# Optimization experiments

Measured on AMD Instinct MI355X. Metric: run time of the kernel, lower is better.

## Reference

```python
import jax, jax.numpy as jnp
import numpy as np
from jax.scipy.special import logsumexp

# ---- static hyperparameters (from init_kwargs) ----
NG, NF, NW = 5, 10, 4
STEP = NG + NF + 1            # 16 signatures per writer mini-batch
T, D_FEAT = 512, 64           # sequence length, embedding dim
N = NW * STEP                 # 64 sequences in the batch
GAMMA = 5.0                   # soft-DTW gamma (bandwidth=0.1 -> int 0 -> no band)
MARGIN, ALPHA, BETA = 1.0, 0.1, 1.0
P_W, R_W = 0.1, 0.1
K_NUM, K_MUL = 5, 2.0
BIG = 1e10                    # stand-in for +inf in the DP boundary


def setup_inputs() -> dict:
    key = jax.random.key(0)
    k1, k2 = jax.random.split(key)
    data = jax.random.normal(k1, (N, T, D_FEAT), dtype=jnp.float32)
    lens = jax.random.randint(k2, (N,), T // 2, T + 1).astype(jnp.int32)
    return {"data": data, "lens": lens}


def _softdtw_batch(A, B, la, lb):
    """Batched soft-DTW (squared-Euclidean cost, softmin with gamma).
    A, B: (P, T, d); la, lb: (P,) int lengths. Returns R[la, lb] per pair.
    Anti-diagonal wavefront scan: diagonal k holds R[i, k-i]."""
    P = A.shape[0]
    a2 = jnp.sum(A * A, -1)
    b2 = jnp.sum(B * B, -1)
    Dm = a2[:, :, None] + b2[:, None, :] - 2.0 * jnp.einsum('ptd,psd->pts', A, B)  # (P,T,T)
    i_idx = jnp.arange(T + 1)
    r0 = jnp.broadcast_to(jnp.where(i_idx == 0, 0.0, BIG), (P, T + 1))  # diag k=0: R[0,0]=0
    r1 = jnp.full((P, T + 1), BIG, dtype=A.dtype)                        # diag k=1: boundary inf

    def shift(x):  # x[i] -> x[i-1], pad row i=0 with BIG
        return jnp.concatenate([jnp.full((P, 1), BIG, x.dtype), x[:, :-1]], axis=1)

    def step(carry, k):
        p2, p1 = carry          # diagonals k-2, k-1, each (P, T+1) indexed by i
        j = k - i_idx
        valid = (i_idx >= 1) & (j >= 1) & (j <= T)
        di = jnp.clip(i_idx - 1, 0, T - 1)
        dj = jnp.clip(j - 1, 0, T - 1)
        cost = Dm[:, di, dj]    # (P, T+1)
        # softmin over (R[i-1,j-1], R[i-1,j], R[i,j-1])
        stack = jnp.stack([shift(p2), shift(p1), p1], 0)
        smin = -GAMMA * logsumexp(-stack / GAMMA, axis=0)
        cur = jnp.where(valid[None, :], cost + smin, BIG)
        return (p1, cur), cur

    ks = jnp.arange(2, 2 * T + 1)
    _, ys = jax.lax.scan(step, (r0, r1), ks)  # (2T-1, P, T+1)
    return ys[la + lb - 2, jnp.arange(P), la]


def _mmd_pair(X, Y):
    """Multi-kernel Gaussian MMD between X, Y: (n, F) each."""
    n = X.shape[0]
    total = jnp.concatenate([X, Y], 0)
    sq = jnp.sum(total * total, -1)
    L2 = sq[:, None] + sq[None, :] - 2.0 * total @ total.T
    m = total.shape[0]
    bw = jnp.sum(L2) / (m * m - m)
    bw = bw / (K_MUL ** (K_NUM // 2))
    bws = bw * (K_MUL ** jnp.arange(K_NUM, dtype=X.dtype))
    K = jnp.sum(jnp.exp(-L2[None, :, :] / bws[:, None, None]), 0)
    return (jnp.mean(K[:n, :n]) + jnp.mean(K[n:, n:])
            - jnp.mean(K[:n, n:]) - jnp.mean(K[n:, :n]))


def _forward(data, lens):
    half = NF // 2
    # all anchor/(positive|negative) pairs across writers, flattened: P = NW*(NG+NF)
    a_idx, b_idx = [], []
    for w in range(NW):
        base = w * STEP
        for j in range(1, STEP):
            a_idx.append(base)
            b_idx.append(base + j)
    a_idx = jnp.array(a_idx)
    b_idx = jnp.array(b_idx)
    la, lb = lens[a_idx], lens[b_idx]
    raw = _softdtw_batch(data[a_idx], data[b_idx], la, lb)
    dist = (raw / (la + lb).astype(data.dtype)).reshape(NW, NG + NF)
    dist_g, dist_n = dist[:, :NG], dist[:, NG:]
    dk = jnp.sqrt(jnp.abs(jnp.mean(dist_g, 1)))       # (NW,)
    dg = dist_g / dk[:, None]
    dn = dist_n / dk[:, None]
    lk_s = jax.nn.relu(dg[:, :, None] + MARGIN - dn[:, None, :half])
    lk_r = jax.nn.relu(dg[:, :, None] + MARGIN - dn[:, None, half:])
    ca = jnp.mean(dg, 1)
    cb = jnp.mean(dn[:, :half], 1)
    intra = jnp.sum(dg - ca[:, None], 1)
    inter = jax.nn.relu(BETA - jnp.abs(ca - cb))
    cnt = jax.lax.stop_gradient(
        (jnp.sum(lk_s > 0, (1, 2)) + jnp.sum(lk_r > 0, (1, 2))).astype(data.dtype))
    lv = (jnp.sum(lk_s, (1, 2)) + jnp.sum(lk_r, (1, 2))) / (cnt + 1.0)
    total_loss = jnp.mean(lv + intra * P_W + inter * R_W)

    # pairwise MMD over writer mini-batches (first 1+NG+half signatures each)
    src, tgt = [], []
    for i in range(NW):
        for j in range(1, NW):
            if i != j:
                src.append(np.arange(STEP * i, STEP * (i + 1) - half))
                tgt.append(np.arange(STEP * j, STEP * (j + 1) - half))
    src = jnp.array(np.stack(src))
    tgt = jnp.array(np.stack(tgt))
    Xs = data[src].reshape(src.shape[0], src.shape[1], -1)  # flatten (T,d) per signature
    Ys = data[tgt].reshape(tgt.shape[0], tgt.shape[1], -1)
    mmds = jax.vmap(_mmd_pair)(Xs, Ys)
    siz = NW * (NW + 1) // 2
    mmds = jnp.concatenate([mmds, jnp.zeros(siz - mmds.shape[0], data.dtype)])
    return total_loss + jnp.max(mmds) * ALPHA


def reference(data, lens):
    return _forward(data, lens)
```

## Files before the change

### kernel.cpp

```cpp
#include <hip/hip_runtime.h>
#include <cstdint>
#include <cstddef>

#define TT 512
#define DFEAT 64
#define NPAIR 60
#define INV_GLN2 0.28853900817779268f
#define NEG_GLN2 -3.4657359027997265f
#define NEGE (-(1 << 29))
#define BM 128
#define BK 64

__constant__ int d_WI[9] = {0,0,0,1,1,2,2,3,3};
__constant__ int d_WJ[9] = {1,2,3,2,3,1,3,1,2};

#if __has_builtin(__builtin_amdgcn_exp2f)
__device__ __forceinline__ float fexp2(float x) { return __builtin_amdgcn_exp2f(x); }
#else
__device__ __forceinline__ float fexp2(float x) { return __expf(0.6931471805599453f * x); }
#endif
#if __has_builtin(__builtin_amdgcn_logf)
__device__ __forceinline__ float flog2(float x) { return __builtin_amdgcn_logf(x); }
#else
__device__ __forceinline__ float flog2(float x) { return 1.4426950408889634f * __logf(x); }
#endif
#if __has_builtin(__builtin_amdgcn_ldexpf)
__device__ __forceinline__ float fldexp(float x, int n) { return __builtin_amdgcn_ldexpf(x, n); }
#else
__device__ __forceinline__ float fldexp(float x, int n) { return ldexpf(x, n); }
#endif
#if __has_builtin(__builtin_amdgcn_frexp_mantf)
__device__ __forceinline__ float fmant(float x) { return __builtin_amdgcn_frexp_mantf(x); }
#else
__device__ __forceinline__ float fmant(float x) { int e; return frexpf(x, &e); }
#endif
#if __has_builtin(__builtin_amdgcn_frexp_expf)
__device__ __forceinline__ int fexpo(float x) { return __builtin_amdgcn_frexp_expf(x); }
#else
__device__ __forceinline__ int fexpo(float x) { int e; frexpf(x, &e); return e; }
#endif

__device__ __forceinline__ unsigned short f2bf(float f) {
  unsigned u = __float_as_uint(f);
  unsigned r = (u + 0x7FFFu + ((u >> 16) & 1u)) >> 16;
  return (unsigned short)r;
}

__global__ __launch_bounds__(256) void norms_kernel(const float* __restrict__ data,
                                                    float* __restrict__ norms) {
  const int g = blockIdx.x * 256 + threadIdx.x;
  const float* __restrict__ row = data + (size_t)g * DFEAT;
  float s = 0.f;
#pragma unroll
  for (int k = 0; k < DFEAT; k += 4) {
    float4 v = *(const float4*)(row + k);
    s += v.x * v.x + v.y * v.y + v.z * v.z + v.w * v.w;
  }
  norms[g] = s;
}

__global__ __launch_bounds__(256) void cost_kernel(const float* __restrict__ data,
                                                   const float* __restrict__ norms,
                                                   const int* __restrict__ lens,
                                                   unsigned short* __restrict__ Dm) {
  const int p = blockIdx.z;
  const int w = p / 15, jb = p % 15 + 1;
  const int la = lens[w * 16], lb = lens[w * 16 + jb];
  const int i0 = blockIdx.y * BM, j0 = blockIdx.x * BM;
  if (i0 >= la || j0 >= lb) return;
  const int an = w * 16, bn = w * 16 + jb;
  const float* __restrict__ A = data + (size_t)an * (TT * DFEAT);
  const float* __restrict__ B = data + (size_t)bn * (TT * DFEAT);

  __shared__ float smem[2 * BK * BM];
  float* As = smem;
  float* Bs = smem + BK * BM;

  const int tid = threadIdx.x;
#pragma unroll
  for (int s2 = 0; s2 < 8; ++s2) {
    const int f = tid + s2 * 256;
    const int row = f >> 4;
    const int k4 = (f & 15) << 2;
    float4 va = *(const float4*)(A + (size_t)(i0 + row) * DFEAT + k4);
    float4 vb = *(const float4*)(B + (size_t)(j0 + row) * DFEAT + k4);
#pragma unroll
    for (int q = 0; q < 4; ++q) {
      const int k = k4 + q;
      const int cp = row ^ (k & 24);
      As[k * BM + cp] = ((const float*)&va)[q];
      Bs[k * BM + cp] = ((const float*)&vb)[q];
    }
  }
  const int ty = tid >> 4, tx = tid & 15;
  const int r0 = ty * 8, c0 = tx * 8;
  float aI[8], bI[8];
#pragma unroll
  for (int q = 0; q < 8; ++q) {
    aI[q] = norms[(size_t)an * TT + i0 + r0 + q] * INV_GLN2;
    bI[q] = norms[(size_t)bn * TT + j0 + c0 + q] * INV_GLN2;
  }
  __syncthreads();

  float acc[8][8] = {};
#pragma unroll 4
  for (int k = 0; k < BK; ++k) {
    const int v = k & 24;
    float af[8], bf8[8];
    *(float4*)&af[0] = *(const float4*)&As[k * BM + (r0 ^ v)];
    *(float4*)&af[4] = *(const float4*)&As[k * BM + (r0 ^ v) + 4];
    *(float4*)&bf8[0] = *(const float4*)&Bs[k * BM + (c0 ^ v)];
    *(float4*)&bf8[4] = *(const float4*)&Bs[k * BM + (c0 ^ v) + 4];
#pragma unroll
    for (int r = 0; r < 8; ++r)
#pragma unroll
      for (int cc = 0; cc < 8; ++cc)
        acc[r][cc] += af[r] * bf8[cc];
  }
  __syncthreads();

  unsigned short* wst = (unsigned short*)smem;
  const float twoInv = 2.0f * INV_GLN2;
#pragma unroll
  for (int cc = 0; cc < 8; ++cc) {
    const int col = c0 + cc;
    unsigned short t8[8];
#pragma unroll
    for (int r = 0; r < 8; ++r) {
      const float x = twoInv * acc[r][cc] - aI[r] - bI[cc];
      t8[r] = f2bf(fexp2(x));
    }
    const int G = ty * 128 + col;
    const int Gs = G ^ (tx & 7);
    const unsigned u0 = (unsigned)t8[0] | ((unsigned)t8[1] << 16);
    const unsigned u1 = (unsigned)t8[2] | ((unsigned)t8[3] << 16);
    const unsigned u2 = (unsigned)t8[4] | ((unsigned)t8[5] << 16);
    const unsigned u3 = (unsigned)t8[6] | ((unsigned)t8[7] << 16);
    uint4 vv; vv.x = u0; vv.y = u1; vv.z = u2; vv.w = u3;
    *(uint4*)&wst[Gs * 8] = vv;
  }
  __syncthreads();
  unsigned short* __restrict__ Dp = Dm + (size_t)p * (TT * TT);
#pragma unroll
  for (int s2 = 0; s2 < 8; ++s2) {
    const int g = tid + s2 * 256;
    const int band = g >> 7, col = g & 127;
    const int Gs = g ^ ((col >> 3) & 7);
    uint4 vv = *(const uint4*)&wst[Gs * 8];
    *(uint4*)(Dp + (size_t)((i0 >> 3) + band) * (TT * 8) + (size_t)(j0 + col) * 8) = vv;
  }
}

__global__ __launch_bounds__(64) void dp_kernel(const unsigned short* __restrict__ Dm,
                                                const int* __restrict__ lens,
                                                float* __restrict__ raw) {
  const int p = blockIdx.x;
  const int w = p / 15, jb = p % 15 + 1;
  const int la = lens[w * 16];
  const int lb = lens[w * 16 + jb];
  const int t = threadIdx.x;
  const int L = (la - 1) >> 3;
  const int dsel = (la - 1) & 7;
  const int s_end = lb + L;

  const unsigned short* __restrict__ base = Dm + (size_t)p * (TT * TT) + (size_t)t * (TT * 8);

  float Xm[8]; int Xe[8];
#pragma unroll
  for (int d = 0; d < 8; ++d) { Xm[d] = 0.f; Xe[d] = NEGE; }
  float upAm = (t == 0) ? 0.5f : 0.f;
  int   upAe = (t == 0) ? 1 : NEGE;
  float upBm = 0.f;
  int   upBe = NEGE;

  auto colidx = [&](int sigma) { return min(max(sigma - t - 1, 0), TT - 1); };
  auto ldcol = [&](int cc) { return *(const uint4*)(base + (size_t)cc * 8); };

  float WA[8], WB[8];
  uint4 q0 = ldcol(colidx(1));
  uint4 q1 = ldcol(colidx(2));
  uint4 RA = ldcol(colidx(3));
  uint4 RB = ldcol(colidx(4));
  {
    const unsigned ua[4] = {q0.x, q0.y, q0.z, q0.w};
    const unsigned ub[4] = {q1.x, q1.y, q1.z, q1.w};
#pragma unroll
    for (int i = 0; i < 4; ++i) {
      WA[2*i]   = __uint_as_float(ua[i] << 16);
      WA[2*i+1] = __uint_as_float(ua[i] & 0xFFFF0000u);
      WB[2*i]   = __uint_as_float(ub[i] << 16);
      WB[2*i+1] = __uint_as_float(ub[i] & 0xFFFF0000u);
    }
  }

  auto decode8 = [&](const uint4& q, float* o) {
    const unsigned u[4] = {q.x, q.y, q.z, q.w};
#pragma unroll
    for (int i = 0; i < 4; ++i) {
      o[2*i]   = __uint_as_float(u[i] << 16);
      o[2*i+1] = __uint_as_float(u[i] & 0xFFFF0000u);
    }
  };

  auto step = [&](int sigma, float* W) {
    const int c = sigma - t;
    if (c >= 1 && c <= TT) {
      float Am = upAm; int Ae = upAe;
      float Bm = upBm; int Be = upBe;
#pragma unroll
      for (int d = 0; d < 8; ++d) {
        const float Cm = Xm[d]; const int Ce = Xe[d];
        const int em = max(max(Ae, Be), Ce);
        const float sum = fldexp(Am, Ae - em) + fldexp(Cm, Ce - em) + fldexp(Bm, Be - em);
        const float pr = W[d] * sum;
        const float nm = fmant(pr);
        const int ne = em + fexpo(pr);
        Am = Cm; Ae = Ce;
        Bm = nm; Be = ne;
        Xm[d] = nm; Xe[d] = ne;
      }
    }
    const float shm = __shfl_up(Xm[7], 1);
    const int she = __shfl_up(Xe[7], 1);
    upAm = upBm; upAe = upBe;
    upBm = (t == 0) ? 0.f : shm;
    upBe = (t == 0) ? NEGE : she;
  };

  int s = 1;
  for (; s + 1 <= s_end; s += 2) {
    step(s, WA);
    decode8(RA, WA);
    RA = ldcol(colidx(s + 4));
    step(s + 1, WB);
    decode8(RB, WB);
    RB = ldcol(colidx(s + 5));
  }
  if (s <= s_end) step(s, WA);

  if (t == L) {
    float xm = Xm[0]; int xe = Xe[0];
#pragma unroll
    for (int d = 1; d < 8; ++d)
      if (dsel == d) { xm = Xm[d]; xe = Xe[d]; }
    raw[p] = NEG_GLN2 * ((float)xe + flog2(xm));
  }
}

__global__ __launch_bounds__(256) void gram_kernel(const float* __restrict__ data,
                                                   float* __restrict__ partials) {
  const int c = blockIdx.x;
  __shared__ float X[44][516];
  const int tid = threadIdx.x;
#pragma unroll
  for (int s = 0; s < 22; ++s) {
    const int f = tid + s * 256;
    const int r = f >> 7;
    const int c4 = (f & 127) << 2;
    const int n = (r / 11) * 16 + (r % 11);
    float4 v = *(const float4*)(data + (size_t)n * (TT * DFEAT) + c * 512 + c4);
    X[r][c4 + 0] = v.x; X[r][c4 + 1] = v.y; X[r][c4 + 2] = v.z; X[r][c4 + 3] = v.w;
  }
  __syncthreads();
  for (int e = tid; e < 44 * 44; e += 256) {
    const int ii = e / 44, jj = e % 44;
    const float* xi = &X[ii][0];
    const float* xj = &X[jj][0];
    float acc = 0.f;
#pragma unroll 8
    for (int k = 0; k < 512; k += 4) {
      float4 u = *(const float4*)(xi + k);
      float4 v = *(const float4*)(xj + k);
      acc += u.x * v.x + u.y * v.y + u.z * v.z + u.w * v.w;
    }
    partials[(size_t)c * (44 * 44) + e] = acc;
  }
}

__device__ __forceinline__ float blockReduceSum(float v, float* sred) {
#pragma unroll
  for (int off = 32; off > 0; off >>= 1) v += __shfl_down(v, off);
  const int tid = threadIdx.x;
  if ((tid & 63) == 0) sred[tid >> 6] = v;
  __syncthreads();
  const float r = sred[0] + sred[1] + sred[2] + sred[3];
  __syncthreads();
  return r;
}

__global__ __launch_bounds__(256) void final_kernel(const float* __restrict__ partials,
                                                    const float* __restrict__ raw,
                                                    const int* __restrict__ lens,
                                                    float* __restrict__ out) {
  __shared__ float G[44 * 44];
  __shared__ float sred[4];
  const int tid = threadIdx.x;
  for (int e = tid; e < 44 * 44; e += 256) {
    float s = 0.f;
    for (int cc = 0; cc < 64; ++cc) s += partials[(size_t)cc * (44 * 44) + e];
    G[e] = s;
  }
  __syncthreads();
  float maxm = 0.f;
  for (int pp = 0; pp < 9; ++pp) {
    const int wi = d_WI[pp], wj = d_WJ[pp];
    float part = 0.f;
    for (int e = tid; e < 484; e += 256) {
      const int p = e / 22, q = e % 22;
      const int vp = (p < 11) ? (wi * 11 + p) : (wj * 11 + p - 11);
      const int vq = (q < 11) ? (wi * 11 + q) : (wj * 11 + q - 11);
      part += G[vp * 44 + vp] + G[vq * 44 + vq] - 2.f * G[vp * 44 + vq];
    }
    const float suml2 = blockReduceSum(part, sred);
    const float bw = suml2 / 462.0f * 0.25f;
    float aXX = 0.f, aXY = 0.f, aYX = 0.f, aYY = 0.f;
    for (int e = tid; e < 484; e += 256) {
      const int p = e / 22, q = e % 22;
      const int vp = (p < 11) ? (wi * 11 + p) : (wj * 11 + p - 11);
      const int vq = (q < 11) ? (wi * 11 + q) : (wj * 11 + q - 11);
      const float l2 = G[vp * 44 + vp] + G[vq * 44 + vq] - 2.f * G[vp * 44 + vq];
      float kk = 0.f;
      float inv = 1.0f / bw;
#pragma unroll
      for (int tkr = 0; tkr < 5; ++tkr) { kk += __expf(-l2 * inv); inv *= 0.5f; }
      const bool pl = p < 11, ql = q < 11;
      aXX += (pl && ql) ? kk : 0.f;
      aXY += (pl && !ql) ? kk : 0.f;
      aYX += (!pl && ql) ? kk : 0.f;
      aYY += (!pl && !ql) ? kk : 0.f;
    }
    const float sXX = blockReduceSum(aXX, sred);
    const float sXY = blockReduceSum(aXY, sred);
    const float sYX = blockReduceSum(aYX, sred);
    const float sYY = blockReduceSum(aYY, sred);
    if (tid == 0) {
      const float mmd = (sXX + sYY - sXY - sYX) / 121.f;
      maxm = fmaxf(maxm, mmd);
    }
  }
  if (tid == 0) {
    float total = 0.f;
    for (int w = 0; w < 4; ++w) {
      const int la0 = lens[w * 16];
      float dist[15];
      for (int q = 0; q < 15; ++q) {
        const int lb = lens[w * 16 + q + 1];
        dist[q] = raw[w * 15 + q] / (float)(la0 + lb);
      }
      const float mg = (dist[0] + dist[1] + dist[2] + dist[3] + dist[4]) * 0.2f;
      const float dk = sqrtf(fabsf(mg));
      float dg[5], dn[10];
      for (int q = 0; q < 5; ++q) dg[q] = dist[q] / dk;
      for (int q = 0; q < 10; ++q) dn[q] = dist[5 + q] / dk;
      float lsum = 0.f, cnt = 0.f;
      for (int a = 0; a < 5; ++a)
        for (int b = 0; b < 10; ++b) {
          const float v = dg[a] + 1.0f - dn[b];
          if (v > 0.f) { lsum += v; cnt += 1.f; }
        }
      const float ca = (dg[0] + dg[1] + dg[2] + dg[3] + dg[4]) * 0.2f;
      const float cb = (dn[0] + dn[1] + dn[2] + dn[3] + dn[4]) * 0.2f;
      float intra = 0.f;
      for (int q = 0; q < 5; ++q) intra += dg[q] - ca;
      const float inter = fmaxf(1.0f - fabsf(ca - cb), 0.f);
      total += lsum / (cnt + 1.0f) + 0.1f * intra + 0.1f * inter;
    }
    total *= 0.25f;
    out[0] = total + 0.1f * maxm;
  }
}

extern "C" void kernel_launch(void* const* d_in, const int* in_sizes, int n_in,
                              void* d_out, int out_size, void* d_ws, size_t ws_size,
                              hipStream_t stream) {
  const float* data = (const float*)d_in[0];
  const int* lens = (const int*)d_in[1];
  float* out = (float*)d_out;
  char* ws = (char*)d_ws;

  const size_t DMB = (size_t)NPAIR * TT * TT * sizeof(unsigned short);
  const size_t RAWB = 1024;
  const size_t PARTB = (size_t)64 * 44 * 44 * sizeof(float);

  unsigned short* Dm = (unsigned short*)ws;
  float* raw = (float*)(ws + DMB);
  float* partials = (float*)(ws + DMB + RAWB);
  float* norms = (float*)(ws + DMB + RAWB + PARTB);

  norms_kernel<<<128, 256, 0, stream>>>(data, norms);
  cost_kernel<<<dim3(4, 4, NPAIR), 256, 0, stream>>>(data, norms, lens, Dm);
  dp_kernel<<<NPAIR, 64, 0, stream>>>(Dm, lens, raw);
  gram_kernel<<<64, 256, 0, stream>>>(data, partials);
  final_kernel<<<1, 256, 0, stream>>>(partials, raw, lens, out);
}
```

Before: 317.4 us.

## Merge DP and Gram kernels into one launch and deepen DP prefetch ring

Fuses the soft-DTW wavefront kernel and the MMD Gram kernel into a single launch: the first 60 blocks run the DP using one wavefront of 64 threads, and the remaining 64 blocks compute Gram partials. The Gram work can then run concurrently on idle CUs while the latency-bound DP proceeds. The DP also replaces its two-deep cost-column prefetch with an eight-entry register ring so global loads are issued further ahead. The costs are more registers per thread and DP blocks that reserve 256 threads and 90KB of shared memory while using only 64 threads, which may limit occupancy.

```diff
diff --git a/kernel.cpp b/kernel.cpp
--- a/kernel.cpp
+++ b/kernel.cpp
@@ -151,129 +151,117 @@
   }
 }
 
-__global__ __launch_bounds__(64) void dp_kernel(const unsigned short* __restrict__ Dm,
-                                                const int* __restrict__ lens,
-                                                float* __restrict__ raw) {
-  const int p = blockIdx.x;
-  const int w = p / 15, jb = p % 15 + 1;
-  const int la = lens[w * 16];
-  const int lb = lens[w * 16 + jb];
-  const int t = threadIdx.x;
-  const int L = (la - 1) >> 3;
-  const int dsel = (la - 1) & 7;
-  const int s_end = lb + L;
-
-  const unsigned short* __restrict__ base = Dm + (size_t)p * (TT * TT) + (size_t)t * (TT * 8);
-
-  float Xm[8]; int Xe[8];
-#pragma unroll
-  for (int d = 0; d < 8; ++d) { Xm[d] = 0.f; Xe[d] = NEGE; }
-  float upAm = (t == 0) ? 0.5f : 0.f;
-  int   upAe = (t == 0) ? 1 : NEGE;
-  float upBm = 0.f;
-  int   upBe = NEGE;
-
-  auto colidx = [&](int sigma) { return min(max(sigma - t - 1, 0), TT - 1); };
-  auto ldcol = [&](int cc) { return *(const uint4*)(base + (size_t)cc * 8); };
-
-  float WA[8], WB[8];
-  uint4 q0 = ldcol(colidx(1));
-  uint4 q1 = ldcol(colidx(2));
-  uint4 RA = ldcol(colidx(3));
-  uint4 RB = ldcol(colidx(4));
-  {
-    const unsigned ua[4] = {q0.x, q0.y, q0.z, q0.w};
-    const unsigned ub[4] = {q1.x, q1.y, q1.z, q1.w};
-#pragma unroll
-    for (int i = 0; i < 4; ++i) {
-      WA[2*i]   = __uint_as_float(ua[i] << 16);
-      WA[2*i+1] = __uint_as_float(ua[i] & 0xFFFF0000u);
-      WB[2*i]   = __uint_as_float(ub[i] << 16);
-      WB[2*i+1] = __uint_as_float(ub[i] & 0xFFFF0000u);
-    }
-  }
-
-  auto decode8 = [&](const uint4& q, float* o) {
-    const unsigned u[4] = {q.x, q.y, q.z, q.w};
-#pragma unroll
-    for (int i = 0; i < 4; ++i) {
-      o[2*i]   = __uint_as_float(u[i] << 16);
-      o[2*i+1] = __uint_as_float(u[i] & 0xFFFF0000u);
-    }
-  };
-
-  auto step = [&](int sigma, float* W) {
-    const int c = sigma - t;
-    if (c >= 1 && c <= TT) {
-      float Am = upAm; int Ae = upAe;
-      float Bm = upBm; int Be = upBe;
-#pragma unroll
-      for (int d = 0; d < 8; ++d) {
-        const float Cm = Xm[d]; const int Ce = Xe[d];
-        const int em = max(max(Ae, Be), Ce);
-        const float sum = fldexp(Am, Ae - em) + fldexp(Cm, Ce - em) + fldexp(Bm, Be - em);
-        const float pr = W[d] * sum;
-        const float nm = fmant(pr);
-        const int ne = em + fexpo(pr);
-        Am = Cm; Ae = Ce;
-        Bm = nm; Be = ne;
-        Xm[d] = nm; Xe[d] = ne;
+__global__ __launch_bounds__(256) void dpgram_kernel(const unsigned short* __restrict__ Dm,
+                                                     const int* __restrict__ lens,
+                                                     float* __restrict__ raw,
+                                                     const float* __restrict__ data,
+                                                     float* __restrict__ partials) {
+  __shared__ float X[44][516];
+  if (blockIdx.x < NPAIR) {
+    if (threadIdx.x >= 64) return;
+    const int p = blockIdx.x;
+    const int w = p / 15, jb = p % 15 + 1;
+    const int la = lens[w * 16];
+    const int lb = lens[w * 16 + jb];
+    const int t = threadIdx.x;
+    const int L = (la - 1) >> 3;
+    const int dsel = (la - 1) & 7;
+    const int s_end = lb + L;
+
+    const unsigned short* __restrict__ base =
+        Dm + (size_t)p * (TT * TT) + (size_t)t * (TT * 8);
+
+    float Xm[8]; int Xe[8];
+#pragma unroll
+    for (int d = 0; d < 8; ++d) { Xm[d] = 0.f; Xe[d] = NEGE; }
+    float upAm = (t == 0) ? 0.5f : 0.f;
+    int   upAe = (t == 0) ? 1 : NEGE;
+    float upBm = 0.f;
+    int   upBe = NEGE;
+
+    auto colidx = [&](int sigma) { return min(max(sigma - t - 1, 0), TT - 1); };
+    auto ldcol = [&](int cc) { return *(const uint4*)(base + (size_t)cc * 8); };
+
+    uint4 ring[8];
+#pragma unroll
+    for (int j = 0; j < 8; ++j) ring[j] = ldcol(colidx(1 + j));
+
+    int s = 1;
+    while (s <= s_end) {
+#pragma unroll
+      for (int j = 0; j < 8; ++j) {
+        if (s <= s_end) {
+          float W8[8];
+          {
+            const unsigned u[4] = {ring[j].x, ring[j].y, ring[j].z, ring[j].w};
+#pragma unroll
+            for (int i = 0; i < 4; ++i) {
+              W8[2 * i]     = __uint_as_float(u[i] << 16);
+              W8[2 * i + 1] = __uint_as_float(u[i] & 0xFFFF0000u);
+            }
+          }
+          ring[j] = ldcol(colidx(s + 8));
+          const int c = s - t;
+          if (c >= 1 && c <= TT) {
+            float Am = upAm; int Ae = upAe;
+            float Bm = upBm; int Be = upBe;
+#pragma unroll
+            for (int d = 0; d < 8; ++d) {
+              const float Cm = Xm[d]; const int Ce = Xe[d];
+              const int em = max(max(Ae, Be), Ce);
+              const float sum = fldexp(Am, Ae - em) + fldexp(Cm, Ce - em) +
+                                fldexp(Bm, Be - em);
+              const float pr = W8[d] * sum;
+              const float nm = fmant(pr);
+              const int ne = em + fexpo(pr);
+              Am = Cm; Ae = Ce;
+              Bm = nm; Be = ne;
+              Xm[d] = nm; Xe[d] = ne;
+            }
+          }
+          const float shm = __shfl_up(Xm[7], 1);
+          const int she = __shfl_up(Xe[7], 1);
+          upAm = upBm; upAe = upBe;
+          upBm = (t == 0) ? 0.f : shm;
+          upBe = (t == 0) ? NEGE : she;
+          ++s;
+        }
       }
     }
-    const float shm = __shfl_up(Xm[7], 1);
-    const int she = __shfl_up(Xe[7], 1);
-    upAm = upBm; upAe = upBe;
-    upBm = (t == 0) ? 0.f : shm;
-    upBe = (t == 0) ? NEGE : she;
-  };
-
-  int s = 1;
-  for (; s + 1 <= s_end; s += 2) {
-    step(s, WA);
-    decode8(RA, WA);
-    RA = ldcol(colidx(s + 4));
-    step(s + 1, WB);
-    decode8(RB, WB);
-    RB = ldcol(colidx(s + 5));
-  }
-  if (s <= s_end) step(s, WA);
-
-  if (t == L) {
-    float xm = Xm[0]; int xe = Xe[0];
-#pragma unroll
-    for (int d = 1; d < 8; ++d)
-      if (dsel == d) { xm = Xm[d]; xe = Xe[d]; }
-    raw[p] = NEG_GLN2 * ((float)xe + flog2(xm));
-  }
-}
-
-__global__ __launch_bounds__(256) void gram_kernel(const float* __restrict__ data,
-                                                   float* __restrict__ partials) {
-  const int c = blockIdx.x;
-  __shared__ float X[44][516];
-  const int tid = threadIdx.x;
-#pragma unroll
-  for (int s = 0; s < 22; ++s) {
-    const int f = tid + s * 256;
-    const int r = f >> 7;
-    const int c4 = (f & 127) << 2;
-    const int n = (r / 11) * 16 + (r % 11);
-    float4 v = *(const float4*)(data + (size_t)n * (TT * DFEAT) + c * 512 + c4);
-    X[r][c4 + 0] = v.x; X[r][c4 + 1] = v.y; X[r][c4 + 2] = v.z; X[r][c4 + 3] = v.w;
-  }
-  __syncthreads();
-  for (int e = tid; e < 44 * 44; e += 256) {
-    const int ii = e / 44, jj = e % 44;
-    const float* xi = &X[ii][0];
-    const float* xj = &X[jj][0];
-    float acc = 0.f;
+
+    if (t == L) {
+      float xm = Xm[0]; int xe = Xe[0];
+#pragma unroll
+      for (int d = 1; d < 8; ++d)
+        if (dsel == d) { xm = Xm[d]; xe = Xe[d]; }
+      raw[p] = NEG_GLN2 * ((float)xe + flog2(xm));
+    }
+  } else {
+    const int c = blockIdx.x - NPAIR;
+    const int tid = threadIdx.x;
+#pragma unroll
+    for (int s = 0; s < 22; ++s) {
+      const int f = tid + s * 256;
+      const int r = f >> 7;
+      const int c4 = (f & 127) << 2;
+      const int n = (r / 11) * 16 + (r % 11);
+      float4 v = *(const float4*)(data + (size_t)n * (TT * DFEAT) + c * 512 + c4);
+      X[r][c4 + 0] = v.x; X[r][c4 + 1] = v.y; X[r][c4 + 2] = v.z; X[r][c4 + 3] = v.w;
+    }
+    __syncthreads();
+    for (int e = tid; e < 44 * 44; e += 256) {
+      const int ii = e / 44, jj = e % 44;
+      const float* xi = &X[ii][0];
+      const float* xj = &X[jj][0];
+      float acc = 0.f;
 #pragma unroll 8
-    for (int k = 0; k < 512; k += 4) {
-      float4 u = *(const float4*)(xi + k);
-      float4 v = *(const float4*)(xj + k);
-      acc += u.x * v.x + u.y * v.y + u.z * v.z + u.w * v.w;
-    }
-    partials[(size_t)c * (44 * 44) + e] = acc;
+      for (int k = 0; k < 512; k += 4) {
+        float4 u = *(const float4*)(xi + k);
+        float4 v = *(const float4*)(xj + k);
+        acc += u.x * v.x + u.y * v.y + u.z * v.z + u.w * v.w;
+      }
+      partials[(size_t)c * (44 * 44) + e] = acc;
+    }
   }
 }
 
@@ -389,7 +377,6 @@
 
   norms_kernel<<<128, 256, 0, stream>>>(data, norms);
   cost_kernel<<<dim3(4, 4, NPAIR), 256, 0, stream>>>(data, norms, lens, Dm);
-  dp_kernel<<<NPAIR, 64, 0, stream>>>(Dm, lens, raw);
-  gram_kernel<<<64, 256, 0, stream>>>(data, partials);
+  dpgram_kernel<<<NPAIR + 64, 256, 0, stream>>>(Dm, lens, raw, data, partials);
   final_kernel<<<1, 256, 0, stream>>>(partials, raw, lens, out);
 }
```

Result: no change. 320.0 us (+0.8%).
